# Performance work log

Measured on AMD Instinct MI355X. Metric: run time of the kernel, lower is better.

The kernel has to match this reference:

```python
import jax, jax.numpy as jnp
import numpy as np

D = 256
H = 8
FFN = 2048
EPS = 1e-5


def _layer_norm(x, g, b):
    m = jnp.mean(x, axis=-1, keepdims=True)
    v = jnp.mean((x - m) ** 2, axis=-1, keepdims=True)
    return (x - m) * jax.lax.rsqrt(v + EPS) * g + b


def _mha(q_in, k_in, v_in, wq, bq, wk, bk, wv, bv, wo, bo, mask):
    B, Sq, _ = q_in.shape
    Sk = k_in.shape[1]
    dh = D // H
    q = (q_in @ wq + bq).reshape(B, Sq, H, dh)
    k = (k_in @ wk + bk).reshape(B, Sk, H, dh)
    v = (v_in @ wv + bv).reshape(B, Sk, H, dh)
    scores = jnp.einsum('bqhd,bkhd->bhqk', q, k) / jnp.sqrt(jnp.float32(dh)).astype(q.dtype)
    if mask is not None:
        scores = scores + mask
    probs = jax.nn.softmax(scores, axis=-1)
    ctx = jnp.einsum('bhqk,bkhd->bqhd', probs, v).reshape(B, Sq, D)
    return ctx @ wo + bo


def setup_inputs() -> dict:
    key = jax.random.key(0)
    ks = jax.random.split(key, 32)
    s = 0.02
    def lin(i, din, dout):
        return jax.random.normal(ks[i], (din, dout), jnp.float32) * s
    inp = {
        'vision_encoder_hidden_states': jax.random.normal(ks[0], (4, 2048, D), jnp.float32),
        'text_encoder_hidden_states': jax.random.normal(ks[1], (4, 1024, D), jnp.float32),
        'vision_encoder_attention_mask': jnp.zeros((4, 1, 1, 2048), jnp.float32),
        'text_encoder_attention_mask': jnp.zeros((4, 1, 1, 1024), jnp.float32),
        'sa_wq': lin(2, D, D), 'sa_bq': jnp.zeros((D,), jnp.float32),
        'sa_wk': lin(3, D, D), 'sa_bk': jnp.zeros((D,), jnp.float32),
        'sa_wv': lin(4, D, D), 'sa_bv': jnp.zeros((D,), jnp.float32),
        'sa_wo': lin(5, D, D), 'sa_bo': jnp.zeros((D,), jnp.float32),
        'ca_wq': lin(6, D, D), 'ca_bq': jnp.zeros((D,), jnp.float32),
        'ca_wk': lin(7, D, D), 'ca_bk': jnp.zeros((D,), jnp.float32),
        'ca_wv': lin(8, D, D), 'ca_bv': jnp.zeros((D,), jnp.float32),
        'ca_wo': lin(9, D, D), 'ca_bo': jnp.zeros((D,), jnp.float32),
        'ln1_g': jnp.ones((D,), jnp.float32), 'ln1_b': jnp.zeros((D,), jnp.float32),
        'ln2_g': jnp.ones((D,), jnp.float32), 'ln2_b': jnp.zeros((D,), jnp.float32),
        'ln3_g': jnp.ones((D,), jnp.float32), 'ln3_b': jnp.zeros((D,), jnp.float32),
        'ln4_g': jnp.ones((D,), jnp.float32), 'ln4_b': jnp.zeros((D,), jnp.float32),
        'fc1_w': lin(10, D, FFN), 'fc1_b': jnp.zeros((FFN,), jnp.float32),
        'fc2_w': lin(11, FFN, D), 'fc2_b': jnp.zeros((D,), jnp.float32),
    }
    return inp


def reference(vision_encoder_hidden_states, text_encoder_hidden_states,
              vision_encoder_attention_mask, text_encoder_attention_mask,
              sa_wq, sa_bq, sa_wk, sa_bk, sa_wv, sa_bv, sa_wo, sa_bo,
              ca_wq, ca_bq, ca_wk, ca_bk, ca_wv, ca_bv, ca_wo, ca_bo,
              ln1_g, ln1_b, ln2_g, ln2_b, ln3_g, ln3_b, ln4_g, ln4_b,
              fc1_w, fc1_b, fc2_w, fc2_b):
    # self-attention over vision queries (dropout = identity in eval)
    residual = vision_encoder_hidden_states
    h = _mha(vision_encoder_hidden_states, vision_encoder_hidden_states,
             vision_encoder_hidden_states,
             sa_wq, sa_bq, sa_wk, sa_bk, sa_wv, sa_bv, sa_wo, sa_bo,
             vision_encoder_attention_mask)
    h = _layer_norm(residual + h, ln1_g, ln1_b)
    # text cross-attention
    res2 = h
    h = _mha(h, text_encoder_hidden_states, text_encoder_hidden_states,
             ca_wq, ca_bq, ca_wk, ca_bk, ca_wv, ca_bv, ca_wo, ca_bo,
             text_encoder_attention_mask)
    h = _layer_norm(res2 + h, ln2_g, ln2_b)
    # third block: residual + dropout(h) -> in eval this is h + h = 2h, then LN
    h = _layer_norm(h + h, ln3_g, ln3_b)
    # FFN
    res = h
    h = jax.nn.relu(h @ fc1_w + fc1_b)
    h = h @ fc2_w + fc2_b
    h = _layer_norm(res + h, ln4_g, ln4_b)
    return h
```

## Files before the change

kernel.cpp:

```cpp
#include <hip/hip_runtime.h>
#include <stdint.h>
#include <stddef.h>

#define HEADS 8
#define DH 32
#define DMODEL 256
#define LN_EPS 1e-5f
#define QSCALE 0.17677669529663687f

typedef unsigned short u16;
typedef __bf16 bf16x8 __attribute__((ext_vector_type(8)));
typedef unsigned short u16x8 __attribute__((ext_vector_type(8)));
typedef float f32x4 __attribute__((ext_vector_type(4)));

static __device__ __forceinline__ u16 bfc(float f) {
    return __builtin_bit_cast(u16, (__bf16)f);
}
static __device__ __forceinline__ bf16x8 ldbf8(const u16* p) {
    return __builtin_bit_cast(bf16x8, *reinterpret_cast<const u16x8*>(p));
}
static __device__ __forceinline__ bf16x8 cvt8(float4 a, float4 b) {
    bf16x8 r;
    r[0] = (__bf16)a.x; r[1] = (__bf16)a.y; r[2] = (__bf16)a.z; r[3] = (__bf16)a.w;
    r[4] = (__bf16)b.x; r[5] = (__bf16)b.y; r[6] = (__bf16)b.z; r[7] = (__bf16)b.w;
    return r;
}

struct TDesc { const float* src; u16* dst; int K; int N; };
struct TArgs { TDesc d[10]; };

__global__ __launch_bounds__(256) void transpose_cvt(TArgs args) {
    TDesc d = args.d[blockIdx.y];
    const int ntx = d.N >> 5;
    const int tiles = (d.K >> 5) * ntx;
    if ((int)blockIdx.x >= tiles) return;
    const int tk = (blockIdx.x / ntx) << 5;
    const int tn = (blockIdx.x % ntx) << 5;
    __shared__ float t[32][33];
    const int lx = threadIdx.x & 31;
    const int ly = threadIdx.x >> 5;
#pragma unroll
    for (int i = 0; i < 4; ++i)
        t[ly + 8 * i][lx] = d.src[(size_t)(tk + ly + 8 * i) * d.N + tn + lx];
    __syncthreads();
#pragma unroll
    for (int i = 0; i < 4; ++i)
        d.dst[(size_t)(tn + ly + 8 * i) * d.K + tk + lx] = bfc(t[lx][ly + 8 * i]);
}

struct Slice { u16* out; const float* bias; int mode; float sc; };

__global__ __launch_bounds__(256) void gemm_xproj(
    const float* __restrict__ Af, const u16* __restrict__ Wt,
    Slice s0, Slice s1, Slice s2, int M, int ntm)
{
    const int lane = threadIdx.x & 63;
    const int wave = threadIdx.x >> 6;
    const int l15 = lane & 15, lhi = lane >> 4;
    const int tm = ((int)blockIdx.x % ntm) * 128;
    const int tn = ((int)blockIdx.x / ntm) * 64;
    const int wm = tm + wave * 32;
    const int sel = tn >> 8;
    const int tl = tn & 255;
    Slice sl = (sel == 0) ? s0 : (sel == 1 ? s1 : s2);

    const f32x4 z4 = {0.f, 0.f, 0.f, 0.f};
    f32x4 acc[2][4];
#pragma unroll
    for (int i = 0; i < 2; ++i)
#pragma unroll
        for (int j = 0; j < 4; ++j) acc[i][j] = z4;

    const float* ar0 = Af + (size_t)(wm + l15) * 256 + lhi * 8;
    const float* ar1 = ar0 + (size_t)16 * 256;
    const u16* b0p = Wt + (size_t)(tn + l15) * 256 + lhi * 8;

    float4 a00 = *(const float4*)(ar0), a01 = *(const float4*)(ar0 + 4);
    float4 a10 = *(const float4*)(ar1), a11 = *(const float4*)(ar1 + 4);
    bf16x8 b[4];
#pragma unroll
    for (int j = 0; j < 4; ++j) b[j] = ldbf8(b0p + (size_t)j * 16 * 256);

#pragma unroll
    for (int k = 32; k < 256; k += 32) {
        float4 n00 = *(const float4*)(ar0 + k), n01 = *(const float4*)(ar0 + k + 4);
        float4 n10 = *(const float4*)(ar1 + k), n11 = *(const float4*)(ar1 + k + 4);
        bf16x8 bn[4];
#pragma unroll
        for (int j = 0; j < 4; ++j) bn[j] = ldbf8(b0p + (size_t)j * 16 * 256 + k);
        bf16x8 a0 = cvt8(a00, a01), a1 = cvt8(a10, a11);
#pragma unroll
        for (int j = 0; j < 4; ++j) {
            acc[0][j] = __builtin_amdgcn_mfma_f32_16x16x32_bf16(a0, b[j], acc[0][j], 0, 0, 0);
            acc[1][j] = __builtin_amdgcn_mfma_f32_16x16x32_bf16(a1, b[j], acc[1][j], 0, 0, 0);
        }
        a00 = n00; a01 = n01; a10 = n10; a11 = n11;
#pragma unroll
        for (int j = 0; j < 4; ++j) b[j] = bn[j];
    }
    {
        bf16x8 a0 = cvt8(a00, a01), a1 = cvt8(a10, a11);
#pragma unroll
        for (int j = 0; j < 4; ++j) {
            acc[0][j] = __builtin_amdgcn_mfma_f32_16x16x32_bf16(a0, b[j], acc[0][j], 0, 0, 0);
            acc[1][j] = __builtin_amdgcn_mfma_f32_16x16x32_bf16(a1, b[j], acc[1][j], 0, 0, 0);
        }
    }

#pragma unroll
    for (int i = 0; i < 2; ++i) {
#pragma unroll
        for (int j = 0; j < 4; ++j) {
            const int col = tl + j * 16 + l15;
            const float bv = sl.bias[col];
            const int row0 = wm + i * 16 + lhi * 4;
            if (sl.mode == 1) {
#pragma unroll
                for (int r = 0; r < 4; ++r)
                    sl.out[(size_t)(row0 + r) * 256 + col] = bfc((acc[i][j][r] + bv) * sl.sc);
            } else {
                ushort4 o = make_ushort4(bfc((acc[i][j][0] + bv) * sl.sc), bfc((acc[i][j][1] + bv) * sl.sc),
                                         bfc((acc[i][j][2] + bv) * sl.sc), bfc((acc[i][j][3] + bv) * sl.sc));
                *reinterpret_cast<ushort4*>(sl.out + (size_t)col * M + row0) = o;
            }
        }
    }
}

template<int MODE, bool RELU>
__global__ __launch_bounds__(256) void gemm_bias(
    const u16* __restrict__ A, const u16* __restrict__ Bt,
    const float* __restrict__ bias, void* __restrict__ Cout,
    int M, int N, int K, int ntm, float osc)
{
    const int lane = threadIdx.x & 63;
    const int wave = threadIdx.x >> 6;
    const int l15 = lane & 15, lhi = lane >> 4;
    const int tm = ((int)blockIdx.x % ntm) * 128;
    const int tn = ((int)blockIdx.x / ntm) * 64;
    const int wm = tm + wave * 32;

    const f32x4 z4 = {0.f, 0.f, 0.f, 0.f};
    f32x4 acc[2][4];
#pragma unroll
    for (int i = 0; i < 2; ++i)
#pragma unroll
        for (int j = 0; j < 4; ++j) acc[i][j] = z4;

    const u16* a0p = A + (size_t)(wm + l15) * K + lhi * 8;
    const u16* a1p = a0p + (size_t)16 * K;
    const u16* b0p = Bt + (size_t)(tn + l15) * K + lhi * 8;

    bf16x8 a0 = ldbf8(a0p), a1 = ldbf8(a1p);
    bf16x8 b[4];
#pragma unroll
    for (int j = 0; j < 4; ++j) b[j] = ldbf8(b0p + (size_t)j * 16 * K);

    for (int k = 32; k < K; k += 32) {
        bf16x8 a0n = ldbf8(a0p + k), a1n = ldbf8(a1p + k);
        bf16x8 bn[4];
#pragma unroll
        for (int j = 0; j < 4; ++j) bn[j] = ldbf8(b0p + (size_t)j * 16 * K + k);
#pragma unroll
        for (int j = 0; j < 4; ++j) {
            acc[0][j] = __builtin_amdgcn_mfma_f32_16x16x32_bf16(a0, b[j], acc[0][j], 0, 0, 0);
            acc[1][j] = __builtin_amdgcn_mfma_f32_16x16x32_bf16(a1, b[j], acc[1][j], 0, 0, 0);
        }
        a0 = a0n; a1 = a1n;
#pragma unroll
        for (int j = 0; j < 4; ++j) b[j] = bn[j];
    }
#pragma unroll
    for (int j = 0; j < 4; ++j) {
        acc[0][j] = __builtin_amdgcn_mfma_f32_16x16x32_bf16(a0, b[j], acc[0][j], 0, 0, 0);
        acc[1][j] = __builtin_amdgcn_mfma_f32_16x16x32_bf16(a1, b[j], acc[1][j], 0, 0, 0);
    }

#pragma unroll
    for (int i = 0; i < 2; ++i) {
#pragma unroll
        for (int j = 0; j < 4; ++j) {
            const int col = tn + j * 16 + l15;
            const float bv = bias[col];
            const int row0 = wm + i * 16 + lhi * 4;
            if (MODE == 0) {
                float* C = (float*)Cout;
#pragma unroll
                for (int r = 0; r < 4; ++r) {
                    float v = acc[i][j][r] + bv;
                    if (RELU) v = fmaxf(v, 0.f);
                    C[(size_t)(row0 + r) * N + col] = v;
                }
            } else {
                u16* C = (u16*)Cout;
#pragma unroll
                for (int r = 0; r < 4; ++r) {
                    float v = acc[i][j][r] + bv;
                    if (RELU) v = fmaxf(v, 0.f);
                    C[(size_t)(row0 + r) * N + col] = bfc(v * osc);
                }
            }
        }
    }
}

__global__ __launch_bounds__(256) void attn_kernel(
    const u16* __restrict__ Qb, const u16* __restrict__ Kb,
    const u16* __restrict__ Vt, const float* __restrict__ mask,
    u16* __restrict__ Ob, int Sq, int Sk, int MkTot)
{
    const int wave = threadIdx.x >> 6;
    const int lane = threadIdx.x & 63;
    const int l15 = lane & 15, lhi = lane >> 4;
    const int nqc = Sq >> 7;
    const int bh = blockIdx.x / nqc;
    const int qc = blockIdx.x % nqc;
    const int b = bh >> 3;
    const int h = bh & 7;
    const int colh = h * DH;
    const int qrow0 = b * Sq + (qc << 7) + wave * 32;
    const int swz = (l15 & 8) << 1;

    __shared__ __align__(16) u16 pt[4][32][72];

    const f32x4 z4 = {0.f, 0.f, 0.f, 0.f};
    bf16x8 qf[2];
    qf[0] = ldbf8(Qb + (size_t)(qrow0 + l15) * DMODEL + colh + lhi * 8);
    qf[1] = ldbf8(Qb + (size_t)(qrow0 + 16 + l15) * DMODEL + colh + lhi * 8);

    f32x4 ctx[2][2] = {{z4, z4}, {z4, z4}};
    float m0 = -1e30f, m1 = -1e30f, ss0 = 0.f, ss1 = 0.f;

    const float* mb = mask + (size_t)b * Sk;
    const u16* kbase = Kb + (size_t)(b * Sk) * DMODEL + colh + lhi * 8;
    const u16* vbase = Vt + (size_t)colh * MkTot + (size_t)b * Sk;

    bf16x8 kf[4], vf[4];
    float4 mk[4];
#pragma unroll
    for (int j = 0; j < 4; ++j)
        kf[j] = ldbf8(kbase + (size_t)(j * 16 + l15) * DMODEL);
#pragma unroll
    for (int ks = 0; ks < 2; ++ks)
#pragma unroll
        for (int dt = 0; dt < 2; ++dt)
            vf[ks * 2 + dt] = ldbf8(vbase + (size_t)(dt * 16 + l15) * MkTot + ks * 32 + lhi * 8);
#pragma unroll
    for (int j = 0; j < 4; ++j)
        mk[j] = *reinterpret_cast<const float4*>(mb + j * 16 + lhi * 4);

    for (int kt = 0; kt < Sk; kt += 64) {
        f32x4 s[2][4];
        __builtin_amdgcn_s_setprio(1);
#pragma unroll
        for (int j = 0; j < 4; ++j) {
            s[0][j] = __builtin_amdgcn_mfma_f32_16x16x32_bf16(kf[j], qf[0], z4, 0, 0, 0);
            s[1][j] = __builtin_amdgcn_mfma_f32_16x16x32_bf16(kf[j], qf[1], z4, 0, 0, 0);
        }
        __builtin_amdgcn_s_setprio(0);

        const int ktn = (kt + 64 < Sk) ? kt + 64 : kt;
        bf16x8 kn[4], vn[4];
        float4 mn[4];
#pragma unroll
        for (int j = 0; j < 4; ++j)
            kn[j] = ldbf8(kbase + (size_t)(ktn + j * 16 + l15) * DMODEL);
#pragma unroll
        for (int ks = 0; ks < 2; ++ks)
#pragma unroll
            for (int dt = 0; dt < 2; ++dt)
                vn[ks * 2 + dt] = ldbf8(vbase + (size_t)(dt * 16 + l15) * MkTot + ktn + ks * 32 + lhi * 8);
#pragma unroll
        for (int j = 0; j < 4; ++j)
            mn[j] = *reinterpret_cast<const float4*>(mb + ktn + j * 16 + lhi * 4);

#pragma unroll
        for (int j = 0; j < 4; ++j) {
            s[0][j][0] += mk[j].x; s[1][j][0] += mk[j].x;
            s[0][j][1] += mk[j].y; s[1][j][1] += mk[j].y;
            s[0][j][2] += mk[j].z; s[1][j][2] += mk[j].z;
            s[0][j][3] += mk[j].w; s[1][j][3] += mk[j].w;
        }

        float mx0 = fmaxf(fmaxf(s[0][0][0], s[0][0][1]), fmaxf(s[0][0][2], s[0][0][3]));
        float mx1 = fmaxf(fmaxf(s[1][0][0], s[1][0][1]), fmaxf(s[1][0][2], s[1][0][3]));
#pragma unroll
        for (int j = 1; j < 4; ++j) {
            mx0 = fmaxf(mx0, fmaxf(fmaxf(s[0][j][0], s[0][j][1]), fmaxf(s[0][j][2], s[0][j][3])));
            mx1 = fmaxf(mx1, fmaxf(fmaxf(s[1][j][0], s[1][j][1]), fmaxf(s[1][j][2], s[1][j][3])));
        }

        if (!__all((mx0 - m0 <= 8.0f) && (mx1 - m1 <= 8.0f))) {
            mx0 = fmaxf(mx0, __shfl_xor(mx0, 16, 64));
            mx0 = fmaxf(mx0, __shfl_xor(mx0, 32, 64));
            mx1 = fmaxf(mx1, __shfl_xor(mx1, 16, 64));
            mx1 = fmaxf(mx1, __shfl_xor(mx1, 32, 64));
            float n0 = fmaxf(m0, mx0), n1 = fmaxf(m1, mx1);
            float c0 = __expf(m0 - n0), c1 = __expf(m1 - n1);
            m0 = n0; m1 = n1; ss0 *= c0; ss1 *= c1;
#pragma unroll
            for (int r = 0; r < 4; ++r) {
                float cc0 = __shfl(c0, lhi * 4 + r, 64);
                float cc1 = __shfl(c1, lhi * 4 + r, 64);
                ctx[0][0][r] *= cc0; ctx[0][1][r] *= cc0;
                ctx[1][0][r] *= cc1; ctx[1][1][r] *= cc1;
            }
        }

        float ps0 = 0.f, ps1 = 0.f;
#pragma unroll
        for (int j = 0; j < 4; ++j)
#pragma unroll
            for (int r = 0; r < 4; ++r) {
                float p0 = __expf(s[0][j][r] - m0);
                float p1 = __expf(s[1][j][r] - m1);
                s[0][j][r] = p0; s[1][j][r] = p1;
                ps0 += p0; ps1 += p1;
            }
        ss0 += ps0; ss1 += ps1;

        asm volatile("" ::: "memory");
#pragma unroll
        for (int i = 0; i < 2; ++i)
#pragma unroll
            for (int j = 0; j < 4; ++j) {
                ushort4 w = make_ushort4(bfc(s[i][j][0]), bfc(s[i][j][1]),
                                         bfc(s[i][j][2]), bfc(s[i][j][3]));
                *reinterpret_cast<ushort4*>(&pt[wave][i * 16 + l15][(j * 16 + lhi * 4) ^ swz]) = w;
            }
        asm volatile("" ::: "memory");

        __builtin_amdgcn_s_setprio(1);
#pragma unroll
        for (int ks = 0; ks < 2; ++ks) {
            bf16x8 pa0 = ldbf8(&pt[wave][l15][(ks * 32 + lhi * 8) ^ swz]);
            bf16x8 pa1 = ldbf8(&pt[wave][16 + l15][(ks * 32 + lhi * 8) ^ swz]);
#pragma unroll
            for (int dt = 0; dt < 2; ++dt) {
                ctx[0][dt] = __builtin_amdgcn_mfma_f32_16x16x32_bf16(pa0, vf[ks * 2 + dt], ctx[0][dt], 0, 0, 0);
                ctx[1][dt] = __builtin_amdgcn_mfma_f32_16x16x32_bf16(pa1, vf[ks * 2 + dt], ctx[1][dt], 0, 0, 0);
            }
        }
        __builtin_amdgcn_s_setprio(0);

#pragma unroll
        for (int j = 0; j < 4; ++j) { kf[j] = kn[j]; vf[j] = vn[j]; mk[j] = mn[j]; }
    }

    ss0 += __shfl_xor(ss0, 16, 64); ss0 += __shfl_xor(ss0, 32, 64);
    ss1 += __shfl_xor(ss1, 16, 64); ss1 += __shfl_xor(ss1, 32, 64);
#pragma unroll
    for (int r = 0; r < 4; ++r) {
        const float i0 = 1.0f / __shfl(ss0, lhi * 4 + r, 64);
        const float i1 = 1.0f / __shfl(ss1, lhi * 4 + r, 64);
        const int row0 = qrow0 + lhi * 4 + r;
#pragma unroll
        for (int dt = 0; dt < 2; ++dt) {
            Ob[(size_t)row0 * DMODEL + colh + dt * 16 + l15] = bfc(ctx[0][dt][r] * i0);
            Ob[(size_t)(row0 + 16) * DMODEL + colh + dt * 16 + l15] = bfc(ctx[1][dt][r] * i1);
        }
    }
}

template<bool DBL, bool WBF>
__global__ __launch_bounds__(256) void ln_kernel(
    const float* __restrict__ X, const float* __restrict__ Res,
    const float* __restrict__ g1p, const float* __restrict__ b1p,
    const float* __restrict__ g2p, const float* __restrict__ b2p,
    float* __restrict__ Of, u16* __restrict__ Oh)
{
    const int lane = threadIdx.x & 63;
    const int row = blockIdx.x * 4 + (threadIdx.x >> 6);
    const size_t base = (size_t)row * DMODEL + lane * 4;
    float4 x = *reinterpret_cast<const float4*>(X + base);
    float4 rr = *reinterpret_cast<const float4*>(Res + base);
    float v[4] = {x.x + rr.x, x.y + rr.y, x.z + rr.z, x.w + rr.w};
    float s = v[0] + v[1] + v[2] + v[3];
    float q = v[0] * v[0] + v[1] * v[1] + v[2] * v[2] + v[3] * v[3];
#pragma unroll
    for (int m = 1; m < 64; m <<= 1) { s += __shfl_xor(s, m, 64); q += __shfl_xor(q, m, 64); }
    float mean = s * (1.0f / DMODEL);
    float rstd = rsqrtf(fmaxf(q * (1.0f / DMODEL) - mean * mean, 0.f) + LN_EPS);
    float4 g = *reinterpret_cast<const float4*>(g1p + lane * 4);
    float4 bb = *reinterpret_cast<const float4*>(b1p + lane * 4);
    float y[4];
    y[0] = (v[0] - mean) * rstd * g.x + bb.x;
    y[1] = (v[1] - mean) * rstd * g.y + bb.y;
    y[2] = (v[2] - mean) * rstd * g.z + bb.z;
    y[3] = (v[3] - mean) * rstd * g.w + bb.w;
    if constexpr (DBL) {
#pragma unroll
        for (int k2 = 0; k2 < 4; ++k2) y[k2] *= 2.0f;
        float s2 = y[0] + y[1] + y[2] + y[3];
        float q2 = y[0] * y[0] + y[1] * y[1] + y[2] * y[2] + y[3] * y[3];
#pragma unroll
        for (int m = 1; m < 64; m <<= 1) { s2 += __shfl_xor(s2, m, 64); q2 += __shfl_xor(q2, m, 64); }
        float mean2 = s2 * (1.0f / DMODEL);
        float rstd2 = rsqrtf(fmaxf(q2 * (1.0f / DMODEL) - mean2 * mean2, 0.f) + LN_EPS);
        float4 g2 = *reinterpret_cast<const float4*>(g2p + lane * 4);
        float4 b2 = *reinterpret_cast<const float4*>(b2p + lane * 4);
        y[0] = (y[0] - mean2) * rstd2 * g2.x + b2.x;
        y[1] = (y[1] - mean2) * rstd2 * g2.y + b2.y;
        y[2] = (y[2] - mean2) * rstd2 * g2.z + b2.z;
        y[3] = (y[3] - mean2) * rstd2 * g2.w + b2.w;
    }
    *reinterpret_cast<float4*>(Of + base) = make_float4(y[0], y[1], y[2], y[3]);
    if constexpr (WBF) {
        ushort4 o = make_ushort4(bfc(y[0]), bfc(y[1]), bfc(y[2]), bfc(y[3]));
        *reinterpret_cast<ushort4*>(Oh + base) = o;
    }
}

extern "C" void kernel_launch(void* const* d_in, const int* in_sizes, int n_in,
                              void* d_out, int out_size, void* d_ws, size_t ws_size,
                              hipStream_t stream) {
    constexpr size_t MB = 1u << 20;
    if (ws_size < 70 * MB) return;

    const float* vis   = (const float*)d_in[0];
    const float* txt   = (const float*)d_in[1];
    const float* vmask = (const float*)d_in[2];
    const float* tmask = (const float*)d_in[3];
    const float* sa_wq = (const float*)d_in[4];  const float* sa_bq = (const float*)d_in[5];
    const float* sa_wk = (const float*)d_in[6];  const float* sa_bk = (const float*)d_in[7];
    const float* sa_wv = (const float*)d_in[8];  const float* sa_bv = (const float*)d_in[9];
    const float* sa_wo = (const float*)d_in[10]; const float* sa_bo = (const float*)d_in[11];
    const float* ca_wq = (const float*)d_in[12]; const float* ca_bq = (const float*)d_in[13];
    const float* ca_wk = (const float*)d_in[14]; const float* ca_bk = (const float*)d_in[15];
    const float* ca_wv = (const float*)d_in[16]; const float* ca_bv = (const float*)d_in[17];
    const float* ca_wo = (const float*)d_in[18]; const float* ca_bo = (const float*)d_in[19];
    const float* ln1_g = (const float*)d_in[20]; const float* ln1_b = (const float*)d_in[21];
    const float* ln2_g = (const float*)d_in[22]; const float* ln2_b = (const float*)d_in[23];
    const float* ln3_g = (const float*)d_in[24]; const float* ln3_b = (const float*)d_in[25];
    const float* ln4_g = (const float*)d_in[26]; const float* ln4_b = (const float*)d_in[27];
    const float* fc1_w = (const float*)d_in[28]; const float* fc1_b = (const float*)d_in[29];
    const float* fc2_w = (const float*)d_in[30]; const float* fc2_b = (const float*)d_in[31];

    const int B = 4, Sq = 2048, St = 1024;
    const int Mq = B * Sq;
    const int Mt = B * St;

    char* ws = (char*)d_ws;
    u16*   q_bf    = (u16*)(ws + 6 * MB);
    u16*   k_bf    = (u16*)(ws + 10 * MB);
    u16*   vt_bf   = (u16*)(ws + 14 * MB);
    u16*   ctx_bf  = (u16*)(ws + 18 * MB);
    u16*   ffn1_bf = (u16*)(ws + 0);
    float* attn_f  = (float*)(ws + 32 * MB);
    float* h1_f    = (float*)(ws + 40 * MB);
    u16*   h1_bf   = (u16*)(ws + 48 * MB);
    float* h3_f    = (float*)(ws + 52 * MB);
    u16*   h3_bf   = (u16*)(ws + 60 * MB);
    u16*   wts     = (u16*)(ws + 64 * MB);
    float* ffn2_f  = attn_f;

    u16* wqkv_t = wts;
    u16* wkv_t  = wqkv_t + 768 * 256;
    u16* cwq_t  = wkv_t + 512 * 256;
    u16* wo_t   = cwq_t + 65536;
    u16* cwo_t  = wo_t + 65536;
    u16* fc1_t  = cwo_t + 65536;
    u16* fc2_t  = fc1_t + 2048 * 256;

    TArgs ta;
    ta.d[0] = {sa_wq, wqkv_t + 0 * 65536, 256, 256};
    ta.d[1] = {sa_wk, wqkv_t + 1 * 65536, 256, 256};
    ta.d[2] = {sa_wv, wqkv_t + 2 * 65536, 256, 256};
    ta.d[3] = {ca_wk, wkv_t + 0 * 65536, 256, 256};
    ta.d[4] = {ca_wv, wkv_t + 1 * 65536, 256, 256};
    ta.d[5] = {ca_wq, cwq_t, 256, 256};
    ta.d[6] = {sa_wo, wo_t, 256, 256};
    ta.d[7] = {ca_wo, cwo_t, 256, 256};
    ta.d[8] = {fc1_w, fc1_t, 256, 2048};
    ta.d[9] = {fc2_w, fc2_t, 2048, 256};
    transpose_cvt<<<dim3(512, 10), 256, 0, stream>>>(ta);

    auto gemm_grid = [](int M, int N) { return dim3((M / 128) * (N / 64)); };

    Slice sq = {q_bf, sa_bq, 1, QSCALE}, sk = {k_bf, sa_bk, 1, 1.f}, sv = {vt_bf, sa_bv, 2, 1.f};
    gemm_xproj<<<dim3((Mq / 128) * 12), 256, 0, stream>>>(vis, wqkv_t, sq, sk, sv, Mq, Mq / 128);
    attn_kernel<<<dim3(B * HEADS * (Sq / 128)), 256, 0, stream>>>(q_bf, k_bf, vt_bf, vmask, ctx_bf, Sq, Sq, Mq);
    gemm_bias<0, false><<<gemm_grid(Mq, 256), 256, 0, stream>>>(ctx_bf, wo_t, sa_bo, attn_f, Mq, 256, 256, Mq / 128, 1.f);
    ln_kernel<false, true><<<dim3(Mq / 4), 256, 0, stream>>>(attn_f, vis, ln1_g, ln1_b, nullptr, nullptr, h1_f, h1_bf);

    Slice ck = {k_bf, ca_bk, 1, 1.f}, cv = {vt_bf, ca_bv, 2, 1.f}, cd = {nullptr, nullptr, 1, 1.f};
    gemm_xproj<<<dim3((Mt / 128) * 8), 256, 0, stream>>>(txt, wkv_t, ck, cv, cd, Mt, Mt / 128);
    gemm_bias<1, false><<<gemm_grid(Mq, 256), 256, 0, stream>>>(h1_bf, cwq_t, ca_bq, q_bf, Mq, 256, 256, Mq / 128, QSCALE);
    attn_kernel<<<dim3(B * HEADS * (Sq / 128)), 256, 0, stream>>>(q_bf, k_bf, vt_bf, tmask, ctx_bf, Sq, St, Mt);
    gemm_bias<0, false><<<gemm_grid(Mq, 256), 256, 0, stream>>>(ctx_bf, cwo_t, ca_bo, attn_f, Mq, 256, 256, Mq / 128, 1.f);
    ln_kernel<true, true><<<dim3(Mq / 4), 256, 0, stream>>>(attn_f, h1_f, ln2_g, ln2_b, ln3_g, ln3_b, h3_f, h3_bf);

    gemm_bias<1, true><<<gemm_grid(Mq, 2048), 256, 0, stream>>>(h3_bf, fc1_t, fc1_b, ffn1_bf, Mq, 2048, 256, Mq / 128, 1.f);
    gemm_bias<0, false><<<gemm_grid(Mq, 256), 256, 0, stream>>>(ffn1_bf, fc2_t, fc2_b, ffn2_f, Mq, 256, 2048, Mq / 128, 1.f);
    ln_kernel<false, false><<<dim3(Mq / 4), 256, 0, stream>>>(ffn2_f, h3_f, ln4_g, ln4_b, nullptr, nullptr, (float*)d_out, nullptr);
}
```

Baseline: 295.4 us.

## Split attention key range across wave pairs and switch softmax to exp2

Each attention block now covers 64 query rows instead of 128, and the two waves sharing a query slice each process half of the key sequence. Partial max, sum and context are then merged through shared memory with a block barrier. This doubles the number of blocks and halves the serial key loop per wave, aiming to raise occupancy and shorten the critical path. The softmax also moves to base-2 exponentials, with log2(e) folded into the Q scale and the mask, and the rescale threshold is widened. The cost is a shared-memory merge epilogue plus a barrier, and the waves with wk=1 sit idle during the final write.

```diff
diff --git a/kernel.cpp b/kernel.cpp
--- a/kernel.cpp
+++ b/kernel.cpp
@@ -6,7 +6,10 @@
 #define DH 32
 #define DMODEL 256
 #define LN_EPS 1e-5f
+#define LOG2E 1.4426950408889634f
 #define QSCALE 0.17677669529663687f
+#define QSCALE2 (QSCALE * LOG2E)
+#define EXP2(x) __builtin_amdgcn_exp2f(x)
 
 typedef unsigned short u16;
 typedef __bf16 bf16x8 __attribute__((ext_vector_type(8)));
@@ -210,30 +213,34 @@
     u16* __restrict__ Ob, int Sq, int Sk, int MkTot)
 {
     const int wave = threadIdx.x >> 6;
+    const int wq = wave >> 1;
+    const int wk = wave & 1;
     const int lane = threadIdx.x & 63;
     const int l15 = lane & 15, lhi = lane >> 4;
-    const int nqc = Sq >> 7;
+    const int nqc = Sq >> 6;
     const int bh = blockIdx.x / nqc;
     const int qc = blockIdx.x % nqc;
     const int b = bh >> 3;
     const int h = bh & 7;
     const int colh = h * DH;
-    const int qrow0 = b * Sq + (qc << 7) + wave * 32;
+    const int qrow0 = b * Sq + (qc << 6) + wq * 32;
     const int swz = (l15 & 8) << 1;
+    const int Sk2 = Sk >> 1;
 
     __shared__ __align__(16) u16 pt[4][32][72];
+    __shared__ __align__(16) float mctx[2][64][16];
+    __shared__ __align__(16) float mst[2][64][4];
 
     const f32x4 z4 = {0.f, 0.f, 0.f, 0.f};
-    bf16x8 qf[2];
-    qf[0] = ldbf8(Qb + (size_t)(qrow0 + l15) * DMODEL + colh + lhi * 8);
-    qf[1] = ldbf8(Qb + (size_t)(qrow0 + 16 + l15) * DMODEL + colh + lhi * 8);
+    const bf16x8 qf0 = ldbf8(Qb + (size_t)(qrow0 + l15) * DMODEL + colh + lhi * 8);
+    const bf16x8 qf1 = ldbf8(Qb + (size_t)(qrow0 + 16 + l15) * DMODEL + colh + lhi * 8);
 
     f32x4 ctx[2][2] = {{z4, z4}, {z4, z4}};
     float m0 = -1e30f, m1 = -1e30f, ss0 = 0.f, ss1 = 0.f;
 
-    const float* mb = mask + (size_t)b * Sk;
-    const u16* kbase = Kb + (size_t)(b * Sk) * DMODEL + colh + lhi * 8;
-    const u16* vbase = Vt + (size_t)colh * MkTot + (size_t)b * Sk;
+    const float* mb = mask + (size_t)b * Sk + wk * Sk2;
+    const u16* kbase = Kb + (size_t)(b * Sk + wk * Sk2) * DMODEL + colh + lhi * 8;
+    const u16* vbase = Vt + (size_t)colh * MkTot + (size_t)b * Sk + wk * Sk2;
 
     bf16x8 kf[4], vf[4];
     float4 mk[4];
@@ -246,20 +253,22 @@
         for (int dt = 0; dt < 2; ++dt)
             vf[ks * 2 + dt] = ldbf8(vbase + (size_t)(dt * 16 + l15) * MkTot + ks * 32 + lhi * 8);
 #pragma unroll
-    for (int j = 0; j < 4; ++j)
-        mk[j] = *reinterpret_cast<const float4*>(mb + j * 16 + lhi * 4);
-
-    for (int kt = 0; kt < Sk; kt += 64) {
+    for (int j = 0; j < 4; ++j) {
+        float4 t0 = *reinterpret_cast<const float4*>(mb + j * 16 + lhi * 4);
+        mk[j] = make_float4(t0.x * LOG2E, t0.y * LOG2E, t0.z * LOG2E, t0.w * LOG2E);
+    }
+
+    for (int kt = 0; kt < Sk2; kt += 64) {
         f32x4 s[2][4];
         __builtin_amdgcn_s_setprio(1);
 #pragma unroll
         for (int j = 0; j < 4; ++j) {
-            s[0][j] = __builtin_amdgcn_mfma_f32_16x16x32_bf16(kf[j], qf[0], z4, 0, 0, 0);
-            s[1][j] = __builtin_amdgcn_mfma_f32_16x16x32_bf16(kf[j], qf[1], z4, 0, 0, 0);
+            s[0][j] = __builtin_amdgcn_mfma_f32_16x16x32_bf16(kf[j], qf0, z4, 0, 0, 0);
+            s[1][j] = __builtin_amdgcn_mfma_f32_16x16x32_bf16(kf[j], qf1, z4, 0, 0, 0);
         }
         __builtin_amdgcn_s_setprio(0);
 
-        const int ktn = (kt + 64 < Sk) ? kt + 64 : kt;
+        const int ktn = (kt + 64 < Sk2) ? kt + 64 : kt;
         bf16x8 kn[4], vn[4];
         float4 mn[4];
 #pragma unroll
@@ -290,13 +299,13 @@
             mx1 = fmaxf(mx1, fmaxf(fmaxf(s[1][j][0], s[1][j][1]), fmaxf(s[1][j][2], s[1][j][3])));
         }
 
-        if (!__all((mx0 - m0 <= 8.0f) && (mx1 - m1 <= 8.0f))) {
+        if (!__all((mx0 - m0 <= 12.0f) && (mx1 - m1 <= 12.0f))) {
             mx0 = fmaxf(mx0, __shfl_xor(mx0, 16, 64));
             mx0 = fmaxf(mx0, __shfl_xor(mx0, 32, 64));
             mx1 = fmaxf(mx1, __shfl_xor(mx1, 16, 64));
             mx1 = fmaxf(mx1, __shfl_xor(mx1, 32, 64));
             float n0 = fmaxf(m0, mx0), n1 = fmaxf(m1, mx1);
-            float c0 = __expf(m0 - n0), c1 = __expf(m1 - n1);
+            float c0 = EXP2(m0 - n0), c1 = EXP2(m1 - n1);
             m0 = n0; m1 = n1; ss0 *= c0; ss1 *= c1;
 #pragma unroll
             for (int r = 0; r < 4; ++r) {
@@ -312,8 +321,8 @@
         for (int j = 0; j < 4; ++j)
 #pragma unroll
             for (int r = 0; r < 4; ++r) {
-                float p0 = __expf(s[0][j][r] - m0);
-                float p1 = __expf(s[1][j][r] - m1);
+                float p0 = EXP2(s[0][j][r] - m0);
+                float p1 = EXP2(s[1][j][r] - m1);
                 s[0][j][r] = p0; s[1][j][r] = p1;
                 ps0 += p0; ps1 += p1;
             }
@@ -349,15 +358,41 @@
 
     ss0 += __shfl_xor(ss0, 16, 64); ss0 += __shfl_xor(ss0, 32, 64);
     ss1 += __shfl_xor(ss1, 16, 64); ss1 += __shfl_xor(ss1, 32, 64);
-#pragma unroll
-    for (int r = 0; r < 4; ++r) {
-        const float i0 = 1.0f / __shfl(ss0, lhi * 4 + r, 64);
-        const float i1 = 1.0f / __shfl(ss1, lhi * 4 + r, 64);
-        const int row0 = qrow0 + lhi * 4 + r;
-#pragma unroll
-        for (int dt = 0; dt < 2; ++dt) {
-            Ob[(size_t)row0 * DMODEL + colh + dt * 16 + l15] = bfc(ctx[0][dt][r] * i0);
-            Ob[(size_t)(row0 + 16) * DMODEL + colh + dt * 16 + l15] = bfc(ctx[1][dt][r] * i1);
+
+    if (wk == 1) {
+#pragma unroll
+        for (int i = 0; i < 2; ++i)
+#pragma unroll
+            for (int dt = 0; dt < 2; ++dt)
+                *reinterpret_cast<f32x4*>(&mctx[wq][lane][(i * 2 + dt) * 4]) = ctx[i][dt];
+        *reinterpret_cast<float4*>(&mst[wq][lane][0]) = make_float4(m0, m1, ss0, ss1);
+    }
+    __syncthreads();
+    if (wk == 0) {
+        float4 stp = *reinterpret_cast<const float4*>(&mst[wq][lane][0]);
+        const float M0 = fmaxf(m0, stp.x), M1 = fmaxf(m1, stp.y);
+        const float c0 = EXP2(m0 - M0), c0p = EXP2(stp.x - M0);
+        const float c1 = EXP2(m1 - M1), c1p = EXP2(stp.y - M1);
+        const float sM0 = ss0 * c0 + stp.z * c0p;
+        const float sM1 = ss1 * c1 + stp.w * c1p;
+#pragma unroll
+        for (int r = 0; r < 4; ++r) {
+            const float cc0  = __shfl(c0,  lhi * 4 + r, 64);
+            const float cc0p = __shfl(c0p, lhi * 4 + r, 64);
+            const float cc1  = __shfl(c1,  lhi * 4 + r, 64);
+            const float cc1p = __shfl(c1p, lhi * 4 + r, 64);
+            const float i0 = 1.0f / __shfl(sM0, lhi * 4 + r, 64);
+            const float i1 = 1.0f / __shfl(sM1, lhi * 4 + r, 64);
+            const int row0 = qrow0 + lhi * 4 + r;
+#pragma unroll
+            for (int dt = 0; dt < 2; ++dt) {
+                const float p0 = mctx[wq][lane][(0 * 2 + dt) * 4 + r];
+                const float p1 = mctx[wq][lane][(1 * 2 + dt) * 4 + r];
+                Ob[(size_t)row0 * DMODEL + colh + dt * 16 + l15] =
+                    bfc((ctx[0][dt][r] * cc0 + p0 * cc0p) * i0);
+                Ob[(size_t)(row0 + 16) * DMODEL + colh + dt * 16 + l15] =
+                    bfc((ctx[1][dt][r] * cc1 + p1 * cc1p) * i1);
+            }
         }
     }
 }
@@ -475,22 +510,20 @@
     ta.d[9] = {fc2_w, fc2_t, 2048, 256};
     transpose_cvt<<<dim3(512, 10), 256, 0, stream>>>(ta);
 
-    auto gemm_grid = [](int M, int N) { return dim3((M / 128) * (N / 64)); };
-
-    Slice sq = {q_bf, sa_bq, 1, QSCALE}, sk = {k_bf, sa_bk, 1, 1.f}, sv = {vt_bf, sa_bv, 2, 1.f};
+    Slice sq = {q_bf, sa_bq, 1, QSCALE2}, sk = {k_bf, sa_bk, 1, 1.f}, sv = {vt_bf, sa_bv, 2, 1.f};
     gemm_xproj<<<dim3((Mq / 128) * 12), 256, 0, stream>>>(vis, wqkv_t, sq, sk, sv, Mq, Mq / 128);
-    attn_kernel<<<dim3(B * HEADS * (Sq / 128)), 256, 0, stream>>>(q_bf, k_bf, vt_bf, vmask, ctx_bf, Sq, Sq, Mq);
-    gemm_bias<0, false><<<gemm_grid(Mq, 256), 256, 0, stream>>>(ctx_bf, wo_t, sa_bo, attn_f, Mq, 256, 256, Mq / 128, 1.f);
+    attn_kernel<<<dim3(B * HEADS * (Sq / 64)), 256, 0, stream>>>(q_bf, k_bf, vt_bf, vmask, ctx_bf, Sq, Sq, Mq);
+    gemm_bias<0, false><<<dim3((Mq / 128) * 4), 256, 0, stream>>>(ctx_bf, wo_t, sa_bo, attn_f, Mq, 256, 256, Mq / 128, 1.f);
     ln_kernel<false, true><<<dim3(Mq / 4), 256, 0, stream>>>(attn_f, vis, ln1_g, ln1_b, nullptr, nullptr, h1_f, h1_bf);
 
     Slice ck = {k_bf, ca_bk, 1, 1.f}, cv = {vt_bf, ca_bv, 2, 1.f}, cd = {nullptr, nullptr, 1, 1.f};
     gemm_xproj<<<dim3((Mt / 128) * 8), 256, 0, stream>>>(txt, wkv_t, ck, cv, cd, Mt, Mt / 128);
-    gemm_bias<1, false><<<gemm_grid(Mq, 256), 256, 0, stream>>>(h1_bf, cwq_t, ca_bq, q_bf, Mq, 256, 256, Mq / 128, QSCALE);
-    attn_kernel<<<dim3(B * HEADS * (Sq / 128)), 256, 0, stream>>>(q_bf, k_bf, vt_bf, tmask, ctx_bf, Sq, St, Mt);
-    gemm_bias<0, false><<<gemm_grid(Mq, 256), 256, 0, stream>>>(ctx_bf, cwo_t, ca_bo, attn_f, Mq, 256, 256, Mq / 128, 1.f);
+    gemm_bias<1, false><<<dim3((Mq / 128) * 4), 256, 0, stream>>>(h1_bf, cwq_t, ca_bq, q_bf, Mq, 256, 256, Mq / 128, QSCALE2);
+    attn_kernel<<<dim3(B * HEADS * (Sq / 64)), 256, 0, stream>>>(q_bf, k_bf, vt_bf, tmask, ctx_bf, Sq, St, Mt);
+    gemm_bias<0, false><<<dim3((Mq / 128) * 4), 256, 0, stream>>>(ctx_bf, cwo_t, ca_bo, attn_f, Mq, 256, 256, Mq / 128, 1.f);
     ln_kernel<true, true><<<dim3(Mq / 4), 256, 0, stream>>>(attn_f, h1_f, ln2_g, ln2_b, ln3_g, ln3_b, h3_f, h3_bf);
 
-    gemm_bias<1, true><<<gemm_grid(Mq, 2048), 256, 0, stream>>>(h3_bf, fc1_t, fc1_b, ffn1_bf, Mq, 2048, 256, Mq / 128, 1.f);
-    gemm_bias<0, false><<<gemm_grid(Mq, 256), 256, 0, stream>>>(ffn1_bf, fc2_t, fc2_b, ffn2_f, Mq, 256, 2048, Mq / 128, 1.f);
+    gemm_bias<1, true><<<dim3((Mq / 128) * 32), 256, 0, stream>>>(h3_bf, fc1_t, fc1_b, ffn1_bf, Mq, 2048, 256, Mq / 128, 1.f);
+    gemm_bias<0, false><<<dim3((Mq / 128) * 4), 256, 0, stream>>>(ffn1_bf, fc2_t, fc2_b, ffn2_f, Mq, 256, 2048, Mq / 128, 1.f);
     ln_kernel<false, false><<<dim3(Mq / 4), 256, 0, stream>>>(ffn2_f, h3_f, ln4_g, ln4_b, nullptr, nullptr, (float*)d_out, nullptr);
 }
```

Measured after the change: 300.1 us. About the same (+1.6%).
